# Performance work log

Measured on AMD Instinct MI355X. Metric: run time of the kernel, lower is better.

Reference implementation:

```python
import jax, jax.numpy as jnp
import numpy as np

N = 50000      # num nodes (== num segments for aggregation)
E = 800000     # num edges
D_IN = 128
D_OUT = 128


def setup_inputs() -> dict:
    key = jax.random.key(0)
    k1, k2, k3, k4, k5, k6 = jax.random.split(key, 6)
    x = jax.random.normal(k1, (N, D_IN), dtype=jnp.float32)
    edge_rows = jax.random.randint(k2, (E,), 0, N, dtype=jnp.int32)
    edge_cols = jax.random.randint(k3, (E,), 0, N, dtype=jnp.int32)
    edge_vals = jax.random.uniform(k4, (E,), dtype=jnp.float32)
    stdv = 1.0 / np.sqrt(D_OUT)
    weight = jax.random.uniform(k5, (D_IN, D_OUT), dtype=jnp.float32, minval=-stdv, maxval=stdv)
    root_weight = jax.random.uniform(k6, (D_IN, D_OUT), dtype=jnp.float32, minval=-stdv, maxval=stdv)
    return {"x": x, "edge_rows": edge_rows, "edge_cols": edge_cols,
            "edge_vals": edge_vals, "weight": weight, "root_weight": root_weight}


def reference(x, edge_rows, edge_cols, edge_vals, weight, root_weight):
    # support = x @ W                                  [N, D_OUT]
    support = jnp.dot(x, weight)
    # out = spmm(adj, support): adj in COO form.
    # message per edge: adj[r, c] * support[c]         [E, D_OUT]
    msgs = support[edge_cols] * edge_vals[:, None]
    agg = jax.ops.segment_sum(msgs, edge_rows, num_segments=N)  # [N, D_OUT]
    # out += x @ W_root  (bias=False configuration)
    return agg + jnp.dot(x, root_weight)
```

## Files before the change

kernel.cpp:

```cpp
#include <hip/hip_runtime.h>

#define D 128
#define NCK 512
#define RPB 64
#define CHUNKCAP 1600
#define BCAP 2048
#define SCANW 1024

typedef short short8 __attribute__((ext_vector_type(8)));
typedef float v4f __attribute__((ext_vector_type(4)));
typedef float float2v __attribute__((ext_vector_type(2)));

static __device__ __forceinline__ unsigned short f2bf(float f) {
    unsigned u = __builtin_bit_cast(unsigned, f);
    u = (u + 0x7FFFu + ((u >> 16) & 1u)) >> 16;
    return (unsigned short)u;
}

__global__ __launch_bounds__(256) void binsort_prep(
    const int* __restrict__ rows, const int* __restrict__ cols,
    const float* __restrict__ vals,
    const float* __restrict__ W, const float* __restrict__ Wr,
    unsigned short* __restrict__ Wt,
    int* __restrict__ cntT, int* __restrict__ offT, int2* __restrict__ sortedB,
    int E, int nbuck, int chunk)
{
    __shared__ int hist[SCANW];
    __shared__ int cur[SCANW];
    __shared__ int2 stg[CHUNKCAP];
    const int t = threadIdx.x, c = blockIdx.x;

    if (t < 64) {
        const int gid = c * 64 + t;
        const int k  = gid >> 8;
        const int nn = gid & 255;
        const float v = (nn < D) ? W[k * D + nn] : Wr[k * D + (nn - D)];
        Wt[nn * D + k] = f2bf(v);
    }
    #pragma unroll
    for (int j = 0; j < SCANW / 256; ++j) hist[t + j * 256] = 0;
    __syncthreads();

    const int base = c * chunk;
    const int endv = min(base + chunk, E);
    for (int e = base + t; e < endv; e += 256)
        atomicAdd(&hist[rows[e] >> 6], 1);
    __syncthreads();

    int cl_[4];
    #pragma unroll
    for (int j = 0; j < 4; ++j) {
        const int idx = t + j * 256;
        cl_[j] = hist[idx];
        if (idx < nbuck) cntT[(size_t)c * nbuck + idx] = cl_[j];
    }
    for (int off = 1; off < SCANW; off <<= 1) {
        int a[4];
        #pragma unroll
        for (int j = 0; j < 4; ++j) {
            const int idx = t + j * 256;
            a[j] = (idx >= off) ? hist[idx - off] : 0;
        }
        __syncthreads();
        #pragma unroll
        for (int j = 0; j < 4; ++j) hist[t + j * 256] += a[j];
        __syncthreads();
    }
    #pragma unroll
    for (int j = 0; j < 4; ++j) {
        const int idx = t + j * 256;
        const int ex = hist[idx] - cl_[j];
        cur[idx] = ex;
        if (idx < nbuck) offT[(size_t)c * nbuck + idx] = ex;
    }
    __syncthreads();

    for (int e = base + t; e < endv; e += 256) {
        const int r  = rows[e];
        const int cc = cols[e];
        const float v = vals[e];
        const int pos = atomicAdd(&cur[r >> 6], 1);
        stg[pos] = make_int2(((r & (RPB - 1)) << 16) | cc, __float_as_int(v));
    }
    __syncthreads();

    const int n = endv - base;
    for (int k = t; k < n; k += 256)
        sortedB[(size_t)base + k] = stg[k];
}

__global__ __launch_bounds__(256) void gemm_dual(
    const float* __restrict__ x, const unsigned short* __restrict__ Wt,
    unsigned short* __restrict__ support, unsigned short* __restrict__ rootbuf,
    int M)
{
    __shared__ unsigned short As[64][136];
    const int tid = threadIdx.x;
    const int w = tid >> 6;
    const int lane = tid & 63;
    const int nl = lane & 15, quad = lane >> 4;
    const int rowBase = (int)blockIdx.x * 64;

    {
        const int r = tid & 63;
        const int seg = tid >> 6;
        const int row = rowBase + r;
        unsigned short tmp[32];
        if (row < M) {
            const float4* src = (const float4*)(x + (size_t)row * D + seg * 32);
            #pragma unroll
            for (int j = 0; j < 8; ++j) {
                const float4 v = src[j];
                tmp[j * 4 + 0] = f2bf(v.x); tmp[j * 4 + 1] = f2bf(v.y);
                tmp[j * 4 + 2] = f2bf(v.z); tmp[j * 4 + 3] = f2bf(v.w);
            }
        } else {
            #pragma unroll
            for (int j = 0; j < 32; ++j) tmp[j] = 0;
        }
        #pragma unroll
        for (int j = 0; j < 4; ++j)
            *(short8*)&As[r][seg * 32 + j * 8] = *(const short8*)&tmp[j * 8];
    }

    short8 bfrag[4][4];
    {
        const unsigned short* wbase = Wt + (size_t)(w * 64 + nl) * D + quad * 8;
        #pragma unroll
        for (int nt = 0; nt < 4; ++nt)
            #pragma unroll
            for (int c = 0; c < 4; ++c)
                bfrag[c][nt] = *(const short8*)(wbase + (size_t)nt * 16 * D + c * 32);
    }
    __syncthreads();

    v4f acc[4][4] = {};
    #pragma unroll
    for (int c = 0; c < 4; ++c) {
        short8 afr[4];
        #pragma unroll
        for (int mt = 0; mt < 4; ++mt)
            afr[mt] = *(const short8*)&As[mt * 16 + nl][c * 32 + quad * 8];
        #pragma unroll
        for (int mt = 0; mt < 4; ++mt)
            #pragma unroll
            for (int nt = 0; nt < 4; ++nt)
                acc[mt][nt] = __builtin_amdgcn_mfma_f32_16x16x32_bf16(
                    afr[mt], bfrag[c][nt], acc[mt][nt], 0, 0, 0);
    }

    const int cbase = (w & 1) * 64;
    unsigned short* dst = (w < 2) ? support : rootbuf;
    #pragma unroll
    for (int mt = 0; mt < 4; ++mt)
        #pragma unroll
        for (int reg = 0; reg < 4; ++reg) {
            const int row = rowBase + mt * 16 + quad * 4 + reg;
            if (row < M) {
                #pragma unroll
                for (int nt = 0; nt < 4; ++nt)
                    dst[(size_t)row * D + cbase + nt * 16 + nl] = f2bf(acc[mt][nt][reg]);
            }
        }
}

__global__ __launch_bounds__(512) void sort_aggregate(
    const int* __restrict__ cntT, const int* __restrict__ offT,
    const int2* __restrict__ sortedB,
    const unsigned short* __restrict__ support,
    const unsigned short* __restrict__ rootbuf,
    float* __restrict__ out, int M, int nbuck, int chunk)
{
    __shared__ int2 stage[BCAP];
    __shared__ unsigned rowList[BCAP];
    __shared__ int csum[NCK];
    __shared__ int offc[NCK];
    __shared__ int rh[RPB];
    __shared__ int rs[RPB + 1];
    __shared__ int rcur[RPB];
    const int b = blockIdx.x, t = threadIdx.x;

    const int mycnt = cntT[(size_t)t * nbuck + b];
    csum[t] = mycnt;
    offc[t] = offT[(size_t)t * nbuck + b];
    __syncthreads();
    for (int off = 1; off < NCK; off <<= 1) {
        const int a = (t >= off) ? csum[t - off] : 0;
        __syncthreads();
        csum[t] += a;
        __syncthreads();
    }
    {
        int dst = csum[t] - mycnt;
        int lim = min(dst + mycnt, BCAP) - dst;
        if (lim < 0) lim = 0;
        const int2* src = sortedB + (size_t)t * chunk + offc[t];
        for (int k = 0; k < lim; ++k) stage[dst + k] = src[k];
    }
    if (t < RPB) rh[t] = 0;
    __syncthreads();

    const int T = min(csum[NCK - 1], BCAP);
    for (int e = t; e < T; e += 512) atomicAdd(&rh[stage[e].x >> 16], 1);
    __syncthreads();
    const int myr = (t < RPB) ? rh[t] : 0;
    for (int off = 1; off < RPB; off <<= 1) {
        int a = 0;
        if (t < RPB && t >= off) a = rh[t - off];
        __syncthreads();
        if (t < RPB) rh[t] += a;
        __syncthreads();
    }
    if (t < RPB) { rs[t] = rh[t] - myr; rcur[t] = rh[t] - myr; }
    if (t == RPB - 1) rs[RPB] = rh[RPB - 1];
    __syncthreads();
    for (int e = t; e < T; e += 512) {
        const int2 ed = stage[e];
        const int rib = ed.x >> 16;
        const int pos = atomicAdd(&rcur[rib], 1);
        rowList[pos] = ((unsigned)f2bf(__int_as_float(ed.y)) << 16)
                     | (unsigned)(ed.x & 0xFFFF);
    }
    __syncthreads();

    const int w = t >> 6, lane = t & 63;
    for (int r = w; r < RPB; r += 8) {
        const int row = b * RPB + r;
        if (row >= M) continue;
        const int s = rs[r], e2 = rs[r + 1];
        float ax = 0.f, ay = 0.f;
        int i = s;

        for (; i + 16 <= e2; i += 16) {
            unsigned d[16];
            #pragma unroll
            for (int j = 0; j < 16; ++j) d[j] = rowList[i + j];
            unsigned p[16];
            #pragma unroll
            for (int j = 0; j < 16; ++j)
                p[j] = *(const unsigned*)(support + (size_t)(d[j] & 0xFFFF) * D + lane * 2);
            #pragma unroll
            for (int j = 0; j < 16; ++j) {
                const float v = __builtin_bit_cast(float, d[j] & 0xFFFF0000u);
                ax += __builtin_bit_cast(float, p[j] << 16) * v;
                ay += __builtin_bit_cast(float, p[j] & 0xFFFF0000u) * v;
            }
        }
        if (i + 8 <= e2) {
            unsigned d[8];
            #pragma unroll
            for (int j = 0; j < 8; ++j) d[j] = rowList[i + j];
            unsigned p[8];
            #pragma unroll
            for (int j = 0; j < 8; ++j)
                p[j] = *(const unsigned*)(support + (size_t)(d[j] & 0xFFFF) * D + lane * 2);
            #pragma unroll
            for (int j = 0; j < 8; ++j) {
                const float v = __builtin_bit_cast(float, d[j] & 0xFFFF0000u);
                ax += __builtin_bit_cast(float, p[j] << 16) * v;
                ay += __builtin_bit_cast(float, p[j] & 0xFFFF0000u) * v;
            }
            i += 8;
        }
        if (i < e2) {
            const int m = e2 - i;
            unsigned d[8];
            #pragma unroll
            for (int j = 0; j < 8; ++j) {
                const int idx = i + (j < m ? j : m - 1);
                const unsigned q = rowList[idx];
                d[j] = (j < m) ? q : (q & 0xFFFFu);
            }
            unsigned p[8];
            #pragma unroll
            for (int j = 0; j < 8; ++j)
                p[j] = *(const unsigned*)(support + (size_t)(d[j] & 0xFFFF) * D + lane * 2);
            #pragma unroll
            for (int j = 0; j < 8; ++j) {
                const float v = __builtin_bit_cast(float, d[j] & 0xFFFF0000u);
                ax += __builtin_bit_cast(float, p[j] << 16) * v;
                ay += __builtin_bit_cast(float, p[j] & 0xFFFF0000u) * v;
            }
        }

        const unsigned pr = *(const unsigned*)(rootbuf + (size_t)row * D + lane * 2);
        float2v ov;
        ov.x = ax + __builtin_bit_cast(float, pr << 16);
        ov.y = ay + __builtin_bit_cast(float, pr & 0xFFFF0000u);
        __builtin_nontemporal_store(ov, (float2v*)(out + (size_t)row * D + lane * 2));
    }
}

extern "C" void kernel_launch(void* const* d_in, const int* in_sizes, int n_in,
                              void* d_out, int out_size, void* d_ws, size_t ws_size,
                              hipStream_t stream) {
    const float* x     = (const float*)d_in[0];
    const int*   erows = (const int*)d_in[1];
    const int*   ecols = (const int*)d_in[2];
    const float* evals = (const float*)d_in[3];
    const float* W     = (const float*)d_in[4];
    const float* Wr    = (const float*)d_in[5];
    float* out = (float*)d_out;

    const int M = in_sizes[0] / D;
    const int E = in_sizes[1];

    const int nbuck = (M + RPB - 1) / RPB;
    const int chunk = (E + NCK - 1) / NCK;

    unsigned short* support = (unsigned short*)d_ws;
    unsigned short* rootbuf = support + (size_t)M * D;
    unsigned short* Wt      = rootbuf + (size_t)M * D;
    int*   cntT    = (int*)(Wt + 2 * D * D);
    int*   offT    = cntT + (size_t)NCK * nbuck;
    int2*  sortedB = (int2*)(offT + (size_t)NCK * nbuck);

    binsort_prep<<<NCK, 256, 0, stream>>>(erows, ecols, evals, W, Wr, Wt,
                                          cntT, offT, sortedB, E, nbuck, chunk);
    gemm_dual<<<(M + 63) / 64, 256, 0, stream>>>(x, Wt, support, rootbuf, M);
    sort_aggregate<<<nbuck, 512, 0, stream>>>(cntT, offT, sortedB,
                                              support, rootbuf, out, M, nbuck, chunk);
}
```

Measured before the change: 159.0 us.

## Merge edge binning and dual GEMM into one launch, pack count/offset

Splits the weight transpose into a tiny separate kernel, then fuses the edge bin-sort and the dual bf16 GEMM into one grid. The first 512 blocks bin edges and the rest compute GEMM tiles, with both sharing one raw shared-memory buffer. This lets the two independent phases run at the same time and drops one kernel boundary. Per-chunk bucket count and offset are packed into a single 32-bit word to halve those reads and writes. The packing assumes both values fit in 16 bits, and the larger shared allocation may reduce occupancy for the GEMM blocks.

```diff
diff --git a/kernel.cpp b/kernel.cpp
--- a/kernel.cpp
+++ b/kernel.cpp
@@ -6,6 +6,7 @@
 #define CHUNKCAP 1600
 #define BCAP 2048
 #define SCANW 1024
+#define RAWB 20992
 
 typedef short short8 __attribute__((ext_vector_type(8)));
 typedef float v4f __attribute__((ext_vector_type(4)));
@@ -17,93 +18,94 @@
     return (unsigned short)u;
 }
 
-__global__ __launch_bounds__(256) void binsort_prep(
+__global__ __launch_bounds__(256) void wt_prep(
+    const float* __restrict__ W, const float* __restrict__ Wr,
+    unsigned short* __restrict__ Wt)
+{
+    const int gid = (int)blockIdx.x * 256 + (int)threadIdx.x;
+    const int k  = gid >> 8;
+    const int nn = gid & 255;
+    const float v = (nn < D) ? W[k * D + nn] : Wr[k * D + (nn - D)];
+    Wt[nn * D + k] = f2bf(v);
+}
+
+__global__ __launch_bounds__(256) void prep_gemm(
     const int* __restrict__ rows, const int* __restrict__ cols,
     const float* __restrict__ vals,
-    const float* __restrict__ W, const float* __restrict__ Wr,
-    unsigned short* __restrict__ Wt,
-    int* __restrict__ cntT, int* __restrict__ offT, int2* __restrict__ sortedB,
-    int E, int nbuck, int chunk)
+    unsigned* __restrict__ pkT, int2* __restrict__ sortedB,
+    const float* __restrict__ x, const unsigned short* __restrict__ Wt,
+    unsigned short* __restrict__ support, unsigned short* __restrict__ rootbuf,
+    int M, int E, int nbuck, int chunk)
 {
-    __shared__ int hist[SCANW];
-    __shared__ int cur[SCANW];
-    __shared__ int2 stg[CHUNKCAP];
-    const int t = threadIdx.x, c = blockIdx.x;
-
-    if (t < 64) {
-        const int gid = c * 64 + t;
-        const int k  = gid >> 8;
-        const int nn = gid & 255;
-        const float v = (nn < D) ? W[k * D + nn] : Wr[k * D + (nn - D)];
-        Wt[nn * D + k] = f2bf(v);
-    }
-    #pragma unroll
-    for (int j = 0; j < SCANW / 256; ++j) hist[t + j * 256] = 0;
-    __syncthreads();
-
-    const int base = c * chunk;
-    const int endv = min(base + chunk, E);
-    for (int e = base + t; e < endv; e += 256)
-        atomicAdd(&hist[rows[e] >> 6], 1);
-    __syncthreads();
-
-    int cl_[4];
-    #pragma unroll
-    for (int j = 0; j < 4; ++j) {
-        const int idx = t + j * 256;
-        cl_[j] = hist[idx];
-        if (idx < nbuck) cntT[(size_t)c * nbuck + idx] = cl_[j];
-    }
-    for (int off = 1; off < SCANW; off <<= 1) {
-        int a[4];
+    __shared__ __align__(16) char raw[RAWB];
+    const int t = threadIdx.x;
+
+    if ((int)blockIdx.x < NCK) {
+        int* hist = (int*)raw;
+        int* cur  = hist + SCANW;
+        int2* stg = (int2*)(raw + 2 * SCANW * 4);
+        const int c = blockIdx.x;
+
+        #pragma unroll
+        for (int j = 0; j < SCANW / 256; ++j) hist[t + j * 256] = 0;
+        __syncthreads();
+
+        const int base = c * chunk;
+        const int endv = min(base + chunk, E);
+        for (int e = base + t; e < endv; e += 256)
+            atomicAdd(&hist[rows[e] >> 6], 1);
+        __syncthreads();
+
+        int cl_[4];
+        #pragma unroll
+        for (int j = 0; j < 4; ++j) cl_[j] = hist[t + j * 256];
+        for (int off = 1; off < SCANW; off <<= 1) {
+            int a[4];
+            #pragma unroll
+            for (int j = 0; j < 4; ++j) {
+                const int idx = t + j * 256;
+                a[j] = (idx >= off) ? hist[idx - off] : 0;
+            }
+            __syncthreads();
+            #pragma unroll
+            for (int j = 0; j < 4; ++j) hist[t + j * 256] += a[j];
+            __syncthreads();
+        }
         #pragma unroll
         for (int j = 0; j < 4; ++j) {
             const int idx = t + j * 256;
-            a[j] = (idx >= off) ? hist[idx - off] : 0;
-        }
-        __syncthreads();
-        #pragma unroll
-        for (int j = 0; j < 4; ++j) hist[t + j * 256] += a[j];
-        __syncthreads();
-    }
-    #pragma unroll
-    for (int j = 0; j < 4; ++j) {
-        const int idx = t + j * 256;
-        const int ex = hist[idx] - cl_[j];
-        cur[idx] = ex;
-        if (idx < nbuck) offT[(size_t)c * nbuck + idx] = ex;
-    }
-    __syncthreads();
-
-    for (int e = base + t; e < endv; e += 256) {
-        const int r  = rows[e];
-        const int cc = cols[e];
-        const float v = vals[e];
-        const int pos = atomicAdd(&cur[r >> 6], 1);
-        stg[pos] = make_int2(((r & (RPB - 1)) << 16) | cc, __float_as_int(v));
-    }
-    __syncthreads();
-
-    const int n = endv - base;
-    for (int k = t; k < n; k += 256)
-        sortedB[(size_t)base + k] = stg[k];
-}
-
-__global__ __launch_bounds__(256) void gemm_dual(
-    const float* __restrict__ x, const unsigned short* __restrict__ Wt,
-    unsigned short* __restrict__ support, unsigned short* __restrict__ rootbuf,
-    int M)
-{
-    __shared__ unsigned short As[64][136];
-    const int tid = threadIdx.x;
-    const int w = tid >> 6;
-    const int lane = tid & 63;
+            const int ex = hist[idx] - cl_[j];
+            cur[idx] = ex;
+            if (idx < nbuck)
+                pkT[(size_t)c * nbuck + idx] =
+                    ((unsigned)cl_[j] << 16) | (unsigned)ex;
+        }
+        __syncthreads();
+
+        for (int e = base + t; e < endv; e += 256) {
+            const int r  = rows[e];
+            const int cc = cols[e];
+            const float v = vals[e];
+            const int pos = atomicAdd(&cur[r >> 6], 1);
+            stg[pos] = make_int2(((r & (RPB - 1)) << 16) | cc, __float_as_int(v));
+        }
+        __syncthreads();
+
+        const int n = endv - base;
+        for (int k = t; k < n; k += 256)
+            sortedB[(size_t)base + k] = stg[k];
+        return;
+    }
+
+    unsigned short (*As)[136] = (unsigned short (*)[136])raw;
+    const int w = t >> 6;
+    const int lane = t & 63;
     const int nl = lane & 15, quad = lane >> 4;
-    const int rowBase = (int)blockIdx.x * 64;
+    const int rowBase = ((int)blockIdx.x - NCK) * 64;
 
     {
-        const int r = tid & 63;
-        const int seg = tid >> 6;
+        const int r = t & 63;
+        const int seg = t >> 6;
         const int row = rowBase + r;
         unsigned short tmp[32];
         if (row < M) {
@@ -165,8 +167,7 @@
 }
 
 __global__ __launch_bounds__(512) void sort_aggregate(
-    const int* __restrict__ cntT, const int* __restrict__ offT,
-    const int2* __restrict__ sortedB,
+    const unsigned* __restrict__ pkT, const int2* __restrict__ sortedB,
     const unsigned short* __restrict__ support,
     const unsigned short* __restrict__ rootbuf,
     float* __restrict__ out, int M, int nbuck, int chunk)
@@ -180,9 +181,10 @@
     __shared__ int rcur[RPB];
     const int b = blockIdx.x, t = threadIdx.x;
 
-    const int mycnt = cntT[(size_t)t * nbuck + b];
+    const unsigned pk = pkT[(size_t)t * nbuck + b];
+    const int mycnt = (int)(pk >> 16);
     csum[t] = mycnt;
-    offc[t] = offT[(size_t)t * nbuck + b];
+    offc[t] = (int)(pk & 0xFFFFu);
     __syncthreads();
     for (int off = 1; off < NCK; off <<= 1) {
         const int a = (t >= off) ? csum[t - off] : 0;
@@ -307,17 +309,18 @@
 
     const int nbuck = (M + RPB - 1) / RPB;
     const int chunk = (E + NCK - 1) / NCK;
+    const int nGemm = (M + 63) / 64;
 
     unsigned short* support = (unsigned short*)d_ws;
     unsigned short* rootbuf = support + (size_t)M * D;
     unsigned short* Wt      = rootbuf + (size_t)M * D;
-    int*   cntT    = (int*)(Wt + 2 * D * D);
-    int*   offT    = cntT + (size_t)NCK * nbuck;
-    int2*  sortedB = (int2*)(offT + (size_t)NCK * nbuck);
-
-    binsort_prep<<<NCK, 256, 0, stream>>>(erows, ecols, evals, W, Wr, Wt,
-                                          cntT, offT, sortedB, E, nbuck, chunk);
-    gemm_dual<<<(M + 63) / 64, 256, 0, stream>>>(x, Wt, support, rootbuf, M);
-    sort_aggregate<<<nbuck, 512, 0, stream>>>(cntT, offT, sortedB,
+    unsigned* pkT   = (unsigned*)(Wt + 2 * D * D);
+    int2*  sortedB  = (int2*)(pkT + (size_t)NCK * nbuck);
+
+    wt_prep<<<128, 256, 0, stream>>>(W, Wr, Wt);
+    prep_gemm<<<NCK + nGemm, 256, 0, stream>>>(
+        erows, ecols, evals, pkT, sortedB, x, Wt, support, rootbuf,
+        M, E, nbuck, chunk);
+    sort_aggregate<<<nbuck, 512, 0, stream>>>(pkT, sortedB,
                                               support, rootbuf, out, M, nbuck, chunk);
 }
```

Measured after the change: 151.4 us. 4.7% less time.
